# Kernel optimization log

Measured on AMD Instinct MI355X. Metric: run time of the kernel, lower is better.

## Reference

```python
import jax, jax.numpy as jnp
import numpy as np
import math

E = 1024      # embedding_nums
H = 16        # head_nums
HD = E // H   # head_embedding_nums = 64
B = 8
S_ENG = 2048  # encoder (K/V) length
S_CHI = 1024  # decoder (Q) length


def setup_inputs() -> dict:
    key = jax.random.key(0)
    k1, k2, k3, k4, k5, k6 = jax.random.split(key, 6)
    scale = 0.02
    return {
        "batch_eng": jax.random.normal(k1, (B, S_ENG, E), dtype=jnp.float32),
        "batch_chi": jax.random.normal(k2, (B, S_CHI, E), dtype=jnp.float32),
        # stacked per-head projections: torch has H separate Linear(E, HD, bias=False)
        "Wq": jax.random.normal(k3, (H, E, HD), dtype=jnp.float32) * scale,
        "Wk": jax.random.normal(k4, (H, E, HD), dtype=jnp.float32) * scale,
        "Wv": jax.random.normal(k5, (H, E, HD), dtype=jnp.float32) * scale,
        "Wo": jax.random.normal(k6, (E, E), dtype=jnp.float32) * scale,
    }


def reference(batch_eng, batch_chi, Wq, Wk, Wv, Wo):
    # Per-head projections, batched over heads instead of a Python loop.
    q = jnp.einsum("bqe,hed->bhqd", batch_chi, Wq)   # [B,H,S_chi,HD]
    k = jnp.einsum("bke,hed->bhkd", batch_eng, Wk)   # [B,H,S_eng,HD]
    v = jnp.einsum("bke,hed->bhkd", batch_eng, Wv)   # [B,H,S_eng,HD]
    scores = jnp.einsum("bhqd,bhkd->bhqk", q, k) / math.sqrt(HD)
    attn = jax.nn.softmax(scores, axis=-1)           # [B,H,S_chi,S_eng]
    out = jnp.einsum("bhqk,bhkd->bhqd", attn, v)     # [B,H,S_chi,HD]
    # concat heads along last dim (matches torch.cat(out, dim=-1) ordering)
    out = out.transpose(0, 2, 1, 3).reshape(B, S_CHI, E)
    return out @ Wo
```

## Files before the change

### kernel.cpp

```cpp
#include <hip/hip_runtime.h>
#include <hip/hip_bf16.h>
#include <stdint.h>

#define E_DIM 1024
#define H_NUM 16
#define HD_DIM 64
#define B_NUM 8
#define SENG 2048
#define SCHI 1024

typedef __attribute__((ext_vector_type(4))) float f32x4;
typedef __attribute__((ext_vector_type(8))) short bf16x8;
typedef __attribute__((ext_vector_type(8))) unsigned short u16x8;
typedef __attribute__((ext_vector_type(4))) unsigned short u16x4;

__device__ __forceinline__ unsigned short f2bf(float f) {
  unsigned int u = __builtin_bit_cast(unsigned int, f);
  u = (u + 0x7fffu + ((u >> 16) & 1u)) >> 16;
  return (unsigned short)u;
}

__device__ __forceinline__ void gload_lds16(const void* g, void* l) {
  __builtin_amdgcn_global_load_lds(
      (const __attribute__((address_space(1))) unsigned int*)g,
      (__attribute__((address_space(3))) unsigned int*)l, 16, 0, 0);
}

__global__ __launch_bounds__(256) void cast_bf16_k(const float* __restrict__ in,
                                                   unsigned short* __restrict__ out,
                                                   int n) {
  int i = (blockIdx.x * 256 + threadIdx.x) * 8;
  if (i >= n) return;
  float4 a = *(const float4*)(in + i);
  float4 b = *(const float4*)(in + i + 4);
  u16x8 v;
  v[0] = f2bf(a.x); v[1] = f2bf(a.y); v[2] = f2bf(a.z); v[3] = f2bf(a.w);
  v[4] = f2bf(b.x); v[5] = f2bf(b.y); v[6] = f2bf(b.z); v[7] = f2bf(b.w);
  *(u16x8*)(out + i) = v;
}

__global__ __launch_bounds__(256) void pack_w_qkv(const float* __restrict__ w,
                                                  unsigned short* __restrict__ wt) {
  int t = blockIdx.x * 256 + threadIdx.x;
  int e = t & 1023;
  int n = t >> 10;
  int h = n >> 6, d = n & 63;
  wt[t] = f2bf(w[(h * E_DIM + e) * HD_DIM + d]);
}

__global__ __launch_bounds__(256) void pack_wo(const float* __restrict__ w,
                                               unsigned short* __restrict__ wt) {
  int t = blockIdx.x * 256 + threadIdx.x;
  int k = t & 1023;
  int n = t >> 10;
  wt[t] = f2bf(w[k * E_DIM + n]);
}

template <int MODE>
__global__ __launch_bounds__(256) void gemm_bt(const unsigned short* __restrict__ A,
                                               const unsigned short* __restrict__ Bt,
                                               void* __restrict__ Cv,
                                               int M, int N, int K) {
  __shared__ unsigned short As[128 * 32];
  __shared__ unsigned short Bs[128 * 32];
  const int tid = threadIdx.x;
  const int w = tid >> 6, lane = tid & 63;
  const int bm = blockIdx.y, bn = blockIdx.x;
  const int wm = w >> 1, wn = w & 1;
  const int rl = lane & 15, gl = lane >> 4;
  f32x4 acc[4][4] = {};

  const int lr = lane >> 2, lc = lane & 3;
  const unsigned short* Ag = A + (size_t)(bm * 128 + w * 32 + lr) * K + lc * 8;
  const unsigned short* Bg = Bt + (size_t)(bn * 128 + w * 32 + lr) * K + lc * 8;
  unsigned short* Asw = As + w * 32 * 32;
  unsigned short* Bsw = Bs + w * 32 * 32;

  for (int kt = 0; kt < K; kt += 32) {
    gload_lds16(Ag + kt, Asw);
    gload_lds16(Ag + kt + 16 * K, Asw + 16 * 32);
    gload_lds16(Bg + kt, Bsw);
    gload_lds16(Bg + kt + 16 * K, Bsw + 16 * 32);
    __syncthreads();
    bf16x8 af[4], bfr[4];
#pragma unroll
    for (int mt = 0; mt < 4; ++mt)
      af[mt] = *(const bf16x8*)&As[(wm * 64 + mt * 16 + rl) * 32 + gl * 8];
#pragma unroll
    for (int nt = 0; nt < 4; ++nt)
      bfr[nt] = *(const bf16x8*)&Bs[(wn * 64 + nt * 16 + rl) * 32 + gl * 8];
#pragma unroll
    for (int mt = 0; mt < 4; ++mt)
#pragma unroll
      for (int nt = 0; nt < 4; ++nt)
        acc[mt][nt] =
            __builtin_amdgcn_mfma_f32_16x16x32_bf16(af[mt], bfr[nt], acc[mt][nt], 0, 0, 0);
    __syncthreads();
  }

#pragma unroll
  for (int mt = 0; mt < 4; ++mt)
#pragma unroll
    for (int nt = 0; nt < 4; ++nt) {
      const int row0 = bm * 128 + wm * 64 + mt * 16 + gl * 4;
      const int col = bn * 128 + wn * 64 + nt * 16 + rl;
      if (MODE == 1) {
        float* C = (float*)Cv;
#pragma unroll
        for (int r = 0; r < 4; ++r) C[(size_t)(row0 + r) * N + col] = acc[mt][nt][r];
      } else if (MODE == 2) {
        unsigned short* Vt = (unsigned short*)Cv;
        const int b = row0 >> 11, kk = row0 & 2047;
        const int h = col >> 6, d = col & 63;
        u16x4 pk;
#pragma unroll
        for (int r = 0; r < 4; ++r) pk[r] = f2bf(acc[mt][nt][r]);
        *(u16x4*)(Vt + (size_t)((b * 16 + h) * 64 + d) * SENG + kk) = pk;
      } else if (MODE == 3) {
        unsigned short* Qh = (unsigned short*)Cv;
        const int b = row0 >> 10, q = row0 & 1023;
        const int h = col >> 6, d = col & 63;
        unsigned short* p = Qh + (((size_t)(b * 16 + h) * SCHI + q) * HD_DIM + d);
#pragma unroll
        for (int r = 0; r < 4; ++r) p[(size_t)r * HD_DIM] = f2bf(acc[mt][nt][r]);
      } else {
        unsigned short* Kh = (unsigned short*)Cv;
        const int b = row0 >> 11, kk = row0 & 2047;
        const int h = col >> 6, d = col & 63;
        unsigned short* p = Kh + (((size_t)(b * 16 + h) * SENG + kk) * HD_DIM + d);
#pragma unroll
        for (int r = 0; r < 4; ++r) p[(size_t)r * HD_DIM] = f2bf(acc[mt][nt][r]);
      }
    }
}

__global__ __launch_bounds__(256) void flash_attn(const unsigned short* __restrict__ Qh,
                                                  const unsigned short* __restrict__ Kh,
                                                  const unsigned short* __restrict__ Vt,
                                                  unsigned short* __restrict__ att) {
  const int bh = blockIdx.x, qb = blockIdx.y;
  const int b = bh >> 4, h = bh & 15;
  const int w = threadIdx.x >> 6, lane = threadIdx.x & 63;
  const int rl = lane & 15, gl = lane >> 4;

  __shared__ unsigned short Ks[2][4096];
  __shared__ unsigned short Vs[2][4096];
  __shared__ unsigned short Plds[4][16][72];

  const unsigned short* Kb = Kh + (size_t)bh * (SENG * HD_DIM);
  const unsigned short* Vb = Vt + (size_t)bh * (HD_DIM * SENG);

  const int q0 = qb * 64 + w * 16;
  const unsigned short* Qp = Qh + ((size_t)bh * SCHI + q0 + rl) * HD_DIM + gl * 8;
  const bf16x8 qf0 = *(const bf16x8*)Qp;
  const bf16x8 qf1 = *(const bf16x8*)(Qp + 32);

  const int lrow = lane >> 3;
  const int scol = ((lane & 7) ^ lrow) << 3;

  f32x4 o[4] = {};
  float m_run[4], l_run[4];
#pragma unroll
  for (int r = 0; r < 4; ++r) { m_run[r] = -1e30f; l_run[r] = 0.f; }
  const float Cs = 0.125f * 1.44269504f;

  auto stage = [&](int k0, int bufi) {
    if (w < 2) {
      const int c0 = w * 4;
#pragma unroll
      for (int j = 0; j < 4; ++j) {
        const int c = c0 + j;
        gload_lds16(Kb + (size_t)(k0 + c * 8 + lrow) * HD_DIM + scol, &Ks[bufi][c * 512]);
      }
    } else {
      const int c0 = (w - 2) * 4;
#pragma unroll
      for (int j = 0; j < 4; ++j) {
        const int c = c0 + j;
        gload_lds16(Vb + (size_t)(c * 8 + lrow) * SENG + k0 + scol, &Vs[bufi][c * 512]);
      }
    }
  };

  stage(0, 0);
  __syncthreads();

  const int xr = (rl & 7) << 4;

  for (int it = 0; it < 32; ++it) {
    const int cur = it & 1;
    if (it < 31) stage((it + 1) * 64, cur ^ 1);

    const char* KsB = (const char*)Ks[cur];
    f32x4 s[4];
#pragma unroll
    for (int t = 0; t < 4; ++t) {
      const char* kb = KsB + (t * 16 + rl) * 128;
      bf16x8 kf0 = *(const bf16x8*)(kb + ((gl * 16) ^ xr));
      bf16x8 kf1 = *(const bf16x8*)(kb + ((64 + gl * 16) ^ xr));
      f32x4 z = {};
      z = __builtin_amdgcn_mfma_f32_16x16x32_bf16(qf0, kf0, z, 0, 0, 0);
      z = __builtin_amdgcn_mfma_f32_16x16x32_bf16(qf1, kf1, z, 0, 0, 0);
      s[t] = z;
    }

    float al[4];
#pragma unroll
    for (int r = 0; r < 4; ++r) {
      float v = fmaxf(fmaxf(s[0][r], s[1][r]), fmaxf(s[2][r], s[3][r]));
      v = fmaxf(v, __shfl_xor(v, 1));
      v = fmaxf(v, __shfl_xor(v, 2));
      v = fmaxf(v, __shfl_xor(v, 4));
      v = fmaxf(v, __shfl_xor(v, 8));
      const float mnew = fmaxf(m_run[r], v * Cs);
      al[r] = exp2f(m_run[r] - mnew);
      m_run[r] = mnew;
    }
#pragma unroll
    for (int r = 0; r < 4; ++r) {
      const float m = m_run[r];
      float p0 = exp2f(fmaf(s[0][r], Cs, -m));
      float p1 = exp2f(fmaf(s[1][r], Cs, -m));
      float p2 = exp2f(fmaf(s[2][r], Cs, -m));
      float p3 = exp2f(fmaf(s[3][r], Cs, -m));
      unsigned short* pr = &Plds[w][gl * 4 + r][0];
      pr[rl]      = f2bf(p0);
      pr[16 + rl] = f2bf(p1);
      pr[32 + rl] = f2bf(p2);
      pr[48 + rl] = f2bf(p3);
      float t = (p0 + p1) + (p2 + p3);
      t += __shfl_xor(t, 1);
      t += __shfl_xor(t, 2);
      t += __shfl_xor(t, 4);
      t += __shfl_xor(t, 8);
      l_run[r] = l_run[r] * al[r] + t;
    }
#pragma unroll
    for (int nt = 0; nt < 4; ++nt)
#pragma unroll
      for (int r = 0; r < 4; ++r) o[nt][r] *= al[r];

    const char* VsB = (const char*)Vs[cur];
#pragma unroll
    for (int ks = 0; ks < 2; ++ks) {
      const bf16x8 pf = *(const bf16x8*)&Plds[w][rl][ks * 32 + gl * 8];
#pragma unroll
      for (int nt = 0; nt < 4; ++nt) {
        const char* vb = VsB + (nt * 16 + rl) * 128;
        bf16x8 vf = *(const bf16x8*)(vb + ((ks * 64 + gl * 16) ^ xr));
        o[nt] = __builtin_amdgcn_mfma_f32_16x16x32_bf16(pf, vf, o[nt], 0, 0, 0);
      }
    }

    __syncthreads();
  }

  unsigned short* ob = att + ((size_t)(b * SCHI + q0)) * E_DIM + h * HD_DIM;
#pragma unroll
  for (int r = 0; r < 4; ++r) {
    const float inv = 1.0f / l_run[r];
#pragma unroll
    for (int nt = 0; nt < 4; ++nt)
      ob[(size_t)(gl * 4 + r) * E_DIM + nt * 16 + rl] = f2bf(o[nt][r] * inv);
  }
}

extern "C" void kernel_launch(void* const* d_in, const int* in_sizes, int n_in,
                              void* d_out, int out_size, void* d_ws, size_t ws_size,
                              hipStream_t stream) {
  const float* eng = (const float*)d_in[0];
  const float* chi = (const float*)d_in[1];
  const float* Wq = (const float*)d_in[2];
  const float* Wk = (const float*)d_in[3];
  const float* Wv = (const float*)d_in[4];
  const float* Wo = (const float*)d_in[5];
  float* out = (float*)d_out;

  char* ws = (char*)d_ws;
  const size_t MB = 1024 * 1024;
  unsigned short* WqT = (unsigned short*)(ws + 0 * MB);
  unsigned short* WkT = (unsigned short*)(ws + 2 * MB);
  unsigned short* WvT = (unsigned short*)(ws + 4 * MB);
  unsigned short* WoT = (unsigned short*)(ws + 6 * MB);
  unsigned short* Xc = (unsigned short*)(ws + 8 * MB);
  unsigned short* Xe = (unsigned short*)(ws + 24 * MB);
  unsigned short* Qh = (unsigned short*)(ws + 56 * MB);
  unsigned short* Kh = (unsigned short*)(ws + 72 * MB);
  unsigned short* Vt = (unsigned short*)(ws + 104 * MB);
  unsigned short* att = Xc;

  pack_w_qkv<<<4096, 256, 0, stream>>>(Wq, WqT);
  pack_w_qkv<<<4096, 256, 0, stream>>>(Wk, WkT);
  pack_w_qkv<<<4096, 256, 0, stream>>>(Wv, WvT);
  pack_wo<<<4096, 256, 0, stream>>>(Wo, WoT);

  cast_bf16_k<<<(B_NUM * SCHI * E_DIM / 8) / 256, 256, 0, stream>>>(chi, Xc, B_NUM * SCHI * E_DIM);
  cast_bf16_k<<<(B_NUM * SENG * E_DIM / 8) / 256, 256, 0, stream>>>(eng, Xe, B_NUM * SENG * E_DIM);

  gemm_bt<3><<<dim3(8, 64), 256, 0, stream>>>(Xc, WqT, (void*)Qh, B_NUM * SCHI, E_DIM, E_DIM);
  gemm_bt<4><<<dim3(8, 128), 256, 0, stream>>>(Xe, WkT, (void*)Kh, B_NUM * SENG, E_DIM, E_DIM);
  gemm_bt<2><<<dim3(8, 128), 256, 0, stream>>>(Xe, WvT, (void*)Vt, B_NUM * SENG, E_DIM, E_DIM);

  flash_attn<<<dim3(128, 16), 256, 0, stream>>>(Qh, Kh, Vt, att);

  gemm_bt<1><<<dim3(8, 64), 256, 0, stream>>>(att, WoT, (void*)out, B_NUM * SCHI, E_DIM, E_DIM);
}
```

Before: 584.5 us.

## Use lazy softmax rescaling, deferred row-sum reduction, and packed bf16 conversion

```diff
diff --git a/kernel.cpp b/kernel.cpp
--- a/kernel.cpp
+++ b/kernel.cpp
@@ -159,9 +159,9 @@
   const int scol = ((lane & 7) ^ lrow) << 3;
 
   f32x4 o[4] = {};
-  float m_run[4], l_run[4];
-#pragma unroll
-  for (int r = 0; r < 4; ++r) { m_run[r] = -1e30f; l_run[r] = 0.f; }
+  float m_run[4], lp[4];
+#pragma unroll
+  for (int r = 0; r < 4; ++r) { m_run[r] = -1e30f; lp[r] = 0.f; }
   const float Cs = 0.125f * 1.44269504f;
 
   auto stage = [&](int k0, int bufi) {
@@ -204,18 +204,29 @@
       s[t] = z;
     }
 
-    float al[4];
-#pragma unroll
-    for (int r = 0; r < 4; ++r) {
-      float v = fmaxf(fmaxf(s[0][r], s[1][r]), fmaxf(s[2][r], s[3][r]));
-      v = fmaxf(v, __shfl_xor(v, 1));
-      v = fmaxf(v, __shfl_xor(v, 2));
-      v = fmaxf(v, __shfl_xor(v, 4));
-      v = fmaxf(v, __shfl_xor(v, 8));
-      const float mnew = fmaxf(m_run[r], v * Cs);
-      al[r] = exp2f(m_run[r] - mnew);
-      m_run[r] = mnew;
-    }
+    float vmax[4];
+#pragma unroll
+    for (int r = 0; r < 4; ++r)
+      vmax[r] = fmaxf(fmaxf(s[0][r], s[1][r]), fmaxf(s[2][r], s[3][r]));
+    const int need =
+        (vmax[0] * Cs > m_run[0] + 8.f) | (vmax[1] * Cs > m_run[1] + 8.f) |
+        (vmax[2] * Cs > m_run[2] + 8.f) | (vmax[3] * Cs > m_run[3] + 8.f);
+    if (__any(need)) {
+#pragma unroll
+      for (int r = 0; r < 4; ++r) {
+        float v = vmax[r];
+        v = fmaxf(v, __shfl_xor(v, 1));
+        v = fmaxf(v, __shfl_xor(v, 2));
+        v = fmaxf(v, __shfl_xor(v, 4));
+        v = fmaxf(v, __shfl_xor(v, 8));
+        const float mnew = fmaxf(m_run[r], v * Cs);
+        const float al = exp2f(m_run[r] - mnew);
+        m_run[r] = mnew;
+        lp[r] *= al;
+        o[0][r] *= al; o[1][r] *= al; o[2][r] *= al; o[3][r] *= al;
+      }
+    }
+
 #pragma unroll
     for (int r = 0; r < 4; ++r) {
       const float m = m_run[r];
@@ -223,22 +234,20 @@
       float p1 = exp2f(fmaf(s[1][r], Cs, -m));
       float p2 = exp2f(fmaf(s[2][r], Cs, -m));
       float p3 = exp2f(fmaf(s[3][r], Cs, -m));
+      unsigned int r01, r23;
+      asm("v_cvt_pk_bf16_f32 %0, %1, %2" : "=v"(r01) : "v"(p0), "v"(p1));
+      asm("v_cvt_pk_bf16_f32 %0, %1, %2" : "=v"(r23) : "v"(p2), "v"(p3));
       unsigned short* pr = &Plds[w][gl * 4 + r][0];
-      pr[rl]      = f2bf(p0);
-      pr[16 + rl] = f2bf(p1);
-      pr[32 + rl] = f2bf(p2);
-      pr[48 + rl] = f2bf(p3);
-      float t = (p0 + p1) + (p2 + p3);
-      t += __shfl_xor(t, 1);
-      t += __shfl_xor(t, 2);
-      t += __shfl_xor(t, 4);
-      t += __shfl_xor(t, 8);
-      l_run[r] = l_run[r] * al[r] + t;
-    }
-#pragma unroll
-    for (int nt = 0; nt < 4; ++nt)
-#pragma unroll
-      for (int r = 0; r < 4; ++r) o[nt][r] *= al[r];
+      pr[rl]      = (unsigned short)r01;
+      pr[16 + rl] = (unsigned short)(r01 >> 16);
+      pr[32 + rl] = (unsigned short)r23;
+      pr[48 + rl] = (unsigned short)(r23 >> 16);
+      const float q0 = __builtin_bit_cast(float, r01 << 16);
+      const float q1 = __builtin_bit_cast(float, r01 & 0xffff0000u);
+      const float q2 = __builtin_bit_cast(float, r23 << 16);
+      const float q3 = __builtin_bit_cast(float, r23 & 0xffff0000u);
+      lp[r] += (q0 + q1) + (q2 + q3);
+    }
 
     const char* VsB = (const char*)Vs[cur];
 #pragma unroll
@@ -258,7 +267,12 @@
   unsigned short* ob = att + ((size_t)(b * SCHI + q0)) * E_DIM + h * HD_DIM;
 #pragma unroll
   for (int r = 0; r < 4; ++r) {
-    const float inv = 1.0f / l_run[r];
+    float t2 = lp[r];
+    t2 += __shfl_xor(t2, 1);
+    t2 += __shfl_xor(t2, 2);
+    t2 += __shfl_xor(t2, 4);
+    t2 += __shfl_xor(t2, 8);
+    const float inv = 1.0f / t2;
 #pragma unroll
     for (int nt = 0; nt < 4; ++nt)
       ob[(size_t)(gl * 4 + r) * E_DIM + nt * 16 + rl] = f2bf(o[nt][r] * inv);
```

New measurement: 517.3 us. 1.13x faster.

## Rewrite flash attention with transposed 32x32 MFMA and register-resident P

Applied to the files above, without the earlier changes.

```diff
diff --git a/kernel.cpp b/kernel.cpp
--- a/kernel.cpp
+++ b/kernel.cpp
@@ -10,14 +10,22 @@
 #define SCHI 1024
 
 typedef __attribute__((ext_vector_type(4))) float f32x4;
+typedef __attribute__((ext_vector_type(16))) float f32x16;
 typedef __attribute__((ext_vector_type(8))) short bf16x8;
 typedef __attribute__((ext_vector_type(8))) unsigned short u16x8;
 typedef __attribute__((ext_vector_type(4))) unsigned short u16x4;
+typedef __attribute__((ext_vector_type(4))) unsigned int u32x4;
 
 __device__ __forceinline__ unsigned short f2bf(float f) {
   unsigned int u = __builtin_bit_cast(unsigned int, f);
   u = (u + 0x7fffu + ((u >> 16) & 1u)) >> 16;
   return (unsigned short)u;
+}
+
+__device__ __forceinline__ unsigned int cvtpk_bf16(float a, float b) {
+  unsigned int r;
+  asm("v_cvt_pk_bf16_f32 %0, %1, %2" : "=v"(r) : "v"(a), "v"(b));
+  return r;
 }
 
 __device__ __forceinline__ void gload_lds16(const void* g, void* l) {
@@ -141,28 +149,22 @@
   const int bh = blockIdx.x, qb = blockIdx.y;
   const int b = bh >> 4, h = bh & 15;
   const int w = threadIdx.x >> 6, lane = threadIdx.x & 63;
-  const int rl = lane & 15, gl = lane >> 4;
+  const int lq = lane & 31, hi = lane >> 5, l7 = lane & 7;
 
   __shared__ unsigned short Ks[2][4096];
   __shared__ unsigned short Vs[2][4096];
-  __shared__ unsigned short Plds[4][16][72];
 
   const unsigned short* Kb = Kh + (size_t)bh * (SENG * HD_DIM);
   const unsigned short* Vb = Vt + (size_t)bh * (HD_DIM * SENG);
 
-  const int q0 = qb * 64 + w * 16;
-  const unsigned short* Qp = Qh + ((size_t)bh * SCHI + q0 + rl) * HD_DIM + gl * 8;
-  const bf16x8 qf0 = *(const bf16x8*)Qp;
-  const bf16x8 qf1 = *(const bf16x8*)(Qp + 32);
+  const int q_row = qb * 128 + w * 32 + lq;
+  const unsigned short* Qp = Qh + ((size_t)bh * SCHI + q_row) * HD_DIM + hi * 8;
+  bf16x8 qf[4];
+#pragma unroll
+  for (int dc = 0; dc < 4; ++dc) qf[dc] = *(const bf16x8*)(Qp + dc * 16);
 
   const int lrow = lane >> 3;
   const int scol = ((lane & 7) ^ lrow) << 3;
-
-  f32x4 o[4] = {};
-  float m_run[4], l_run[4];
-#pragma unroll
-  for (int r = 0; r < 4; ++r) { m_run[r] = -1e30f; l_run[r] = 0.f; }
-  const float Cs = 0.125f * 1.44269504f;
 
   auto stage = [&](int k0, int bufi) {
     if (w < 2) {
@@ -182,87 +184,111 @@
     }
   };
 
+  int koff[4];
+#pragma unroll
+  for (int dc = 0; dc < 4; ++dc)
+    koff[dc] = lq * 128 + (((2 * dc + hi) ^ l7) << 4);
+  int voff[2][4];
+#pragma unroll
+  for (int dt = 0; dt < 2; ++dt)
+#pragma unroll
+    for (int kc = 0; kc < 4; ++kc)
+      voff[dt][kc] = (dt * 32 + lq) * 128 + (((2 * kc + hi) ^ l7) << 4);
+
+  f32x16 o[2] = {};
+  float m_run = -1e30f, lp = 0.f;
+  const float Cs = 0.125f * 1.44269504f;
+
   stage(0, 0);
   __syncthreads();
-
-  const int xr = (rl & 7) << 4;
 
   for (int it = 0; it < 32; ++it) {
     const int cur = it & 1;
     if (it < 31) stage((it + 1) * 64, cur ^ 1);
 
     const char* KsB = (const char*)Ks[cur];
-    f32x4 s[4];
-#pragma unroll
-    for (int t = 0; t < 4; ++t) {
-      const char* kb = KsB + (t * 16 + rl) * 128;
-      bf16x8 kf0 = *(const bf16x8*)(kb + ((gl * 16) ^ xr));
-      bf16x8 kf1 = *(const bf16x8*)(kb + ((64 + gl * 16) ^ xr));
-      f32x4 z = {};
-      z = __builtin_amdgcn_mfma_f32_16x16x32_bf16(qf0, kf0, z, 0, 0, 0);
-      z = __builtin_amdgcn_mfma_f32_16x16x32_bf16(qf1, kf1, z, 0, 0, 0);
-      s[t] = z;
-    }
-
-    float al[4];
-#pragma unroll
-    for (int r = 0; r < 4; ++r) {
-      float v = fmaxf(fmaxf(s[0][r], s[1][r]), fmaxf(s[2][r], s[3][r]));
-      v = fmaxf(v, __shfl_xor(v, 1));
-      v = fmaxf(v, __shfl_xor(v, 2));
-      v = fmaxf(v, __shfl_xor(v, 4));
-      v = fmaxf(v, __shfl_xor(v, 8));
-      const float mnew = fmaxf(m_run[r], v * Cs);
-      al[r] = exp2f(m_run[r] - mnew);
-      m_run[r] = mnew;
-    }
-#pragma unroll
-    for (int r = 0; r < 4; ++r) {
-      const float m = m_run[r];
-      float p0 = exp2f(fmaf(s[0][r], Cs, -m));
-      float p1 = exp2f(fmaf(s[1][r], Cs, -m));
-      float p2 = exp2f(fmaf(s[2][r], Cs, -m));
-      float p3 = exp2f(fmaf(s[3][r], Cs, -m));
-      unsigned short* pr = &Plds[w][gl * 4 + r][0];
-      pr[rl]      = f2bf(p0);
-      pr[16 + rl] = f2bf(p1);
-      pr[32 + rl] = f2bf(p2);
-      pr[48 + rl] = f2bf(p3);
-      float t = (p0 + p1) + (p2 + p3);
-      t += __shfl_xor(t, 1);
-      t += __shfl_xor(t, 2);
-      t += __shfl_xor(t, 4);
-      t += __shfl_xor(t, 8);
-      l_run[r] = l_run[r] * al[r] + t;
-    }
-#pragma unroll
-    for (int nt = 0; nt < 4; ++nt)
-#pragma unroll
-      for (int r = 0; r < 4; ++r) o[nt][r] *= al[r];
+    f32x16 st0 = {}, st1 = {};
+#pragma unroll
+    for (int dc = 0; dc < 4; ++dc) {
+      bf16x8 kf0 = *(const bf16x8*)(KsB + koff[dc]);
+      bf16x8 kf1 = *(const bf16x8*)(KsB + 4096 + koff[dc]);
+      st0 = __builtin_amdgcn_mfma_f32_32x32x16_bf16(kf0, qf[dc], st0, 0, 0, 0);
+      st1 = __builtin_amdgcn_mfma_f32_32x32x16_bf16(kf1, qf[dc], st1, 0, 0, 0);
+    }
+
+    float mbuf[16];
+#pragma unroll
+    for (int r = 0; r < 16; ++r) mbuf[r] = fmaxf(st0[r], st1[r]);
+#pragma unroll
+    for (int s2 = 8; s2 > 0; s2 >>= 1)
+#pragma unroll
+      for (int i = 0; i < 8; ++i)
+        if (i < s2) mbuf[i] = fmaxf(mbuf[i], mbuf[i + s2]);
+    float v = mbuf[0];
+    v = fmaxf(v, __shfl_xor(v, 32));
+    if (__any(v * Cs > m_run + 8.f)) {
+      const float mnew = fmaxf(m_run, v * Cs);
+      const float al = exp2f(m_run - mnew);
+      m_run = mnew;
+      lp *= al;
+      o[0] *= al;
+      o[1] *= al;
+    }
+
+    float p0a[16], p1a[16];
+#pragma unroll
+    for (int r = 0; r < 16; ++r) p0a[r] = exp2f(fmaf(st0[r], Cs, -m_run));
+#pragma unroll
+    for (int r = 0; r < 16; ++r) p1a[r] = exp2f(fmaf(st1[r], Cs, -m_run));
+    float sbuf[16];
+#pragma unroll
+    for (int r = 0; r < 16; ++r) sbuf[r] = p0a[r] + p1a[r];
+#pragma unroll
+    for (int s2 = 8; s2 > 0; s2 >>= 1)
+#pragma unroll
+      for (int i = 0; i < 8; ++i)
+        if (i < s2) sbuf[i] += sbuf[i + s2];
+    lp += sbuf[0];
+
+    bf16x8 pa[4];
+#pragma unroll
+    for (int kc = 0; kc < 4; ++kc) {
+      const float* ps = (kc < 2) ? p0a : p1a;
+      const int base = (kc & 1) * 8;
+      unsigned int ua = cvtpk_bf16(ps[base + 0], ps[base + 1]);
+      unsigned int ub = cvtpk_bf16(ps[base + 2], ps[base + 3]);
+      unsigned int va = cvtpk_bf16(ps[base + 4], ps[base + 5]);
+      unsigned int vb = cvtpk_bf16(ps[base + 6], ps[base + 7]);
+      asm("v_permlane32_swap_b32 %0, %1" : "+v"(ua), "+v"(va));
+      asm("v_permlane32_swap_b32 %0, %1" : "+v"(ub), "+v"(vb));
+      pa[kc] = __builtin_bit_cast(bf16x8, (u32x4){ua, ub, va, vb});
+    }
 
     const char* VsB = (const char*)Vs[cur];
 #pragma unroll
-    for (int ks = 0; ks < 2; ++ks) {
-      const bf16x8 pf = *(const bf16x8*)&Plds[w][rl][ks * 32 + gl * 8];
-#pragma unroll
-      for (int nt = 0; nt < 4; ++nt) {
-        const char* vb = VsB + (nt * 16 + rl) * 128;
-        bf16x8 vf = *(const bf16x8*)(vb + ((ks * 64 + gl * 16) ^ xr));
-        o[nt] = __builtin_amdgcn_mfma_f32_16x16x32_bf16(pf, vf, o[nt], 0, 0, 0);
+    for (int kc = 0; kc < 4; ++kc) {
+#pragma unroll
+      for (int dt = 0; dt < 2; ++dt) {
+        bf16x8 vf = *(const bf16x8*)(VsB + voff[dt][kc]);
+        o[dt] = __builtin_amdgcn_mfma_f32_32x32x16_bf16(vf, pa[kc], o[dt], 0, 0, 0);
       }
     }
 
     __syncthreads();
   }
 
-  unsigned short* ob = att + ((size_t)(b * SCHI + q0)) * E_DIM + h * HD_DIM;
-#pragma unroll
-  for (int r = 0; r < 4; ++r) {
-    const float inv = 1.0f / l_run[r];
-#pragma unroll
-    for (int nt = 0; nt < 4; ++nt)
-      ob[(size_t)(gl * 4 + r) * E_DIM + nt * 16 + rl] = f2bf(o[nt][r] * inv);
-  }
+  const float lf = lp + __shfl_xor(lp, 32);
+  const float inv = 1.0f / lf;
+  unsigned short* ob = att + (size_t)(b * SCHI + q_row) * E_DIM + h * HD_DIM;
+#pragma unroll
+  for (int dt = 0; dt < 2; ++dt)
+#pragma unroll
+    for (int j = 0; j < 4; ++j) {
+      u16x4 pk;
+#pragma unroll
+      for (int i = 0; i < 4; ++i) pk[i] = f2bf(o[dt][4 * j + i] * inv);
+      *(u16x4*)(ob + dt * 32 + 8 * j + 4 * hi) = pk;
+    }
 }
 
 extern "C" void kernel_launch(void* const* d_in, const int* in_sizes, int n_in,
@@ -301,7 +327,7 @@
   gemm_bt<4><<<dim3(8, 128), 256, 0, stream>>>(Xe, WkT, (void*)Kh, B_NUM * SENG, E_DIM, E_DIM);
   gemm_bt<2><<<dim3(8, 128), 256, 0, stream>>>(Xe, WvT, (void*)Vt, B_NUM * SENG, E_DIM, E_DIM);
 
-  flash_attn<<<dim3(128, 16), 256, 0, stream>>>(Qh, Kh, Vt, att);
+  flash_attn<<<dim3(128, 8), 256, 0, stream>>>(Qh, Kh, Vt, att);
 
   gemm_bt<1><<<dim3(8, 64), 256, 0, stream>>>(att, WoT, (void*)out, B_NUM * SCHI, E_DIM, E_DIM);
 }
```

After: 505.0 us. 13.6% less time.
